# Kernel optimization log

Hardware: AMD Instinct MI355X
Metric: run time of the kernel (lower is better)

## Reference

```python
import jax, jax.numpy as jnp
import numpy as np

# --- reconstructed config / key constants (from init_kwargs) ---
SCALES = (8, 16, 32)                      # patch sizes tiling H, W
TEMPORAL_WINDOWS = (0, 250, 500, 750, 1000)
KEY_INT = 0x5D1CE5                        # deterministic int derived from watermark_key+model_id
BASE_STRENGTH = 0.05
HASH_MOD = 10007
TWO_PI = 6.2831853


def _watermark_bias_map(latent, timestep):
    """Vectorized equivalent of the per-scale / per-patch Python loops.

    For each scale p: tile HxW into (H/p)x(W/p) patches, pool latent over
    (batch, channel, patch) -> scalar per patch, combine with a keyed integer
    hash phase into g in [-1,1], scale by a per-(scale,timestep) strength, and
    paint the constant bias over each patch region (the spatial mask).
    Returns a [H, W] bias map broadcastable over [B, C, H, W].
    """
    B, C, H, W = latent.shape
    # temporal bucket (timestep is a static Python int)
    bucket = int(np.searchsorted(np.asarray(TEMPORAL_WINDOWS), timestep, side='right') - 1)
    total = jnp.zeros((H, W), dtype=latent.dtype)
    for p in SCALES:
        gh, gw = H // p, W // p
        # pooled features per patch: mean over batch, channels, and patch pixels -> [gh, gw]
        pooled = latent.reshape(B, C, gh, p, gw, p).mean(axis=(0, 1, 3, 5))
        # keyed hash phase per patch (top-left coords i*p, j*p)
        base = (KEY_INT * 2654435761 + p * 97 + bucket * 139) % HASH_MOD
        i = (jnp.arange(gh, dtype=jnp.int32) * (p * 131))[:, None]
        j = (jnp.arange(gw, dtype=jnp.int32) * (p * 137))[None, :]
        h = (base + i + j) % HASH_MOD                           # [gh, gw] int
        phase = h.astype(latent.dtype) * (TWO_PI / HASH_MOD)
        g = jnp.cos(pooled * 3.0 + phase)                       # g_value in [-1, 1]
        strength = np.float32(BASE_STRENGTH / np.sqrt(p) * np.exp(-timestep / 1000.0))
        # broadcast patch-constant bias over the full spatial mask region
        total = total + jnp.repeat(jnp.repeat(g * strength, p, axis=0), p, axis=1)
    return total


def setup_inputs() -> dict:
    key = jax.random.key(0)
    k1, k2 = jax.random.split(key)
    B, C, H, W = 64, 4, 256, 256
    noise = jax.random.normal(k1, (B, C, H, W), dtype=jnp.float32)
    latent = jax.random.normal(k2, (B, C, H, W), dtype=jnp.float32)
    return {"noise": noise, "latent": latent, "timestep": 500}


def reference(noise, latent, timestep):
    bias = _watermark_bias_map(latent, timestep)        # [H, W]
    return noise + bias[None, None, :, :]               # [B, C, H, W]
```

## Files before the change

### kernel.cpp

```cpp
#include <hip/hip_runtime.h>
#include <hip/hip_bf16.h>

static constexpr int KEY_MUL =
    (int)((6102245ULL * 2654435761ULL) % 10007ULL);
static constexpr int HASH_MOD = 10007;

typedef float f32x4 __attribute__((ext_vector_type(4)));

__global__ __launch_bounds__(256, 8) void pool_kernel32(
    const float* __restrict__ latent, float* __restrict__ ws_partial) {
  const int ch = blockIdx.x;
  const int pr = blockIdx.y >> 1;
  const int half = blockIdx.y & 1;
  const int t = threadIdx.x;
  const int cl = t & 31;
  const int rg = t >> 5;

  const float4* base = reinterpret_cast<const float4*>(latent);
  float4 v[8];
#pragma unroll
  for (int pl = 0; pl < 8; ++pl)
    v[pl] = base[(size_t)(ch * 8 + pl) * 16384 + (pr * 8 + rg) * 64 +
                 half * 32 + cl];
  float acc = 0.0f;
#pragma unroll
  for (int pl = 0; pl < 8; ++pl) acc += (v[pl].x + v[pl].y) + (v[pl].z + v[pl].w);
  acc += __shfl_xor(acc, 1, 64);

  __shared__ float lds[8][16];
  if ((cl & 1) == 0) lds[rg][cl >> 1] = acc;
  __syncthreads();
  if (t < 16) {
    float s = ((lds[0][t] + lds[1][t]) + (lds[2][t] + lds[3][t])) +
              ((lds[4][t] + lds[5][t]) + (lds[6][t] + lds[7][t]));
    ws_partial[(pr * 32 + half * 16 + t) * 32 + ch] = s;
  }
}

template <int NCH>
__global__ __launch_bounds__(256) void pool_kernel_legacy(
    const float* __restrict__ latent, float* __restrict__ ws_partial) {
  constexpr int PPC = 256 / NCH;
  const int pr = blockIdx.y, ch = blockIdx.x, t = threadIdx.x;
  const int cl = t & 63, rg = t >> 6;
  float acc = 0.0f;
  const float4* base = reinterpret_cast<const float4*>(latent);
#pragma unroll 8
  for (int pl = 0; pl < PPC; ++pl) {
    const float4* prow = base + (size_t)(ch * PPC + pl) * 16384;
#pragma unroll
    for (int rr = 0; rr < 2; ++rr) {
      float4 v = prow[(pr * 8 + rg + rr * 4) * 64 + cl];
      acc += (v.x + v.y) + (v.z + v.w);
    }
  }
  acc += __shfl_xor(acc, 1, 64);
  __shared__ float lds[4][32];
  if ((cl & 1) == 0) lds[rg][cl >> 1] = acc;
  __syncthreads();
  if (t < 32) {
    float s = (lds[0][t] + lds[1][t]) + (lds[2][t] + lds[3][t]);
    ws_partial[(pr * 32 + t) * NCH + ch] = s;
  }
}

template <int NCH>
__global__ __launch_bounds__(256, 8) void bias_add_kernel(
    const float* __restrict__ noise, const float* __restrict__ ws_partial,
    const int* __restrict__ tstep, float* __restrict__ out) {
  const int t = threadIdx.x;
  const int b = blockIdx.x;
  const int q = b & 7;

  __shared__ float s8[128];
  __shared__ float btot[128];

  const size_t slab = (size_t)(b >> 3) * 16384 + (size_t)q * 2048;
  const f32x4* __restrict__ n4 = reinterpret_cast<const f32x4*>(noise) + slab;
  f32x4* __restrict__ o4 = reinterpret_cast<f32x4*>(out) + slab;

  f32x4 v[8];
#pragma unroll
  for (int k = 0; k < 8; ++k) v[k] = n4[k * 256 + t];

  const int ts = *tstep;

  if (t < 128) {
    const int lr = t >> 5;
    const int lc = t & 31;
    const int patch = (4 * q + lr) * 32 + lc;
    float s = 0.0f;
    if constexpr (NCH >= 4) {
      const float4* p4 =
          reinterpret_cast<const float4*>(ws_partial) + patch * (NCH / 4);
#pragma unroll
      for (int c = 0; c < NCH / 4; ++c) {
        float4 w = p4[c];
        s += (w.x + w.y) + (w.z + w.w);
      }
    } else {
#pragma unroll
      for (int c = 0; c < NCH; ++c) s += ws_partial[patch * NCH + c];
    }
    s8[t] = s;
  }
  __syncthreads();

  if (t < 128) {
    const int lr = t >> 5;
    const int lc = t & 31;
    const int pr = 4 * q + lr;

    int bucket = -1;
    const int wins[5] = {0, 250, 500, 750, 1000};
#pragma unroll
    for (int k = 0; k < 5; ++k) bucket += (ts >= wins[k]) ? 1 : 0;

    const float expo = expf((float)(-ts) * 0.001f);
    const float phase_k = (float)(6.2831853 / 10007.0);

    float bias = 0.0f;
    {
      const int bb = (KEY_MUL + 8 * 97 + bucket * 139) % HASH_MOD;
      const int h = (bb + pr * (8 * 131) + lc * (8 * 137)) % HASH_MOD;
      const float pooled = s8[t] * (1.0f / 16384.0f);
      bias += cosf(pooled * 3.0f + (float)h * phase_k) *
              (0.0176776695296637f * expo);
    }
    {
      const int bb = (KEY_MUL + 16 * 97 + bucket * 139) % HASH_MOD;
      const int h =
          (bb + (pr >> 1) * (16 * 131) + (lc >> 1) * (16 * 137)) % HASH_MOD;
      const int r0 = (lr & ~1) * 32, c0 = lc & ~1;
      const float s = (s8[r0 + c0] + s8[r0 + c0 + 1]) +
                      (s8[r0 + 32 + c0] + s8[r0 + 32 + c0 + 1]);
      const float pooled = s * (1.0f / 65536.0f);
      bias += cosf(pooled * 3.0f + (float)h * phase_k) *
              (0.0125f * expo);
    }
    {
      const int bb = (KEY_MUL + 32 * 97 + bucket * 139) % HASH_MOD;
      const int h = (bb + q * (32 * 131) + (lc >> 2) * (32 * 137)) % HASH_MOD;
      const int c0 = lc & ~3;
      float s = 0.0f;
#pragma unroll
      for (int di = 0; di < 4; ++di)
#pragma unroll
        for (int dj = 0; dj < 4; ++dj) s += s8[di * 32 + c0 + dj];
      const float pooled = s * (1.0f / 262144.0f);
      bias += cosf(pooled * 3.0f + (float)h * phase_k) *
              (0.00883883476483184f * expo);
    }
    btot[t] = bias;
  }
  __syncthreads();

  {
    const int c8 = (t & 63) >> 1;
    const int r0 = t >> 6;
#pragma unroll
    for (int k = 0; k < 8; ++k) {
      const int lrow = k * 4 + r0;
      const float bs = btot[(lrow >> 3) * 32 + c8];
      f32x4 w = v[k];
      w.x += bs; w.y += bs; w.z += bs; w.w += bs;
      o4[k * 256 + t] = w;
    }
  }
}

extern "C" void kernel_launch(void* const* d_in, const int* in_sizes, int n_in,
                              void* d_out, int out_size, void* d_ws, size_t ws_size,
                              hipStream_t stream) {
  const float* noise  = (const float*)d_in[0];
  const float* latent = (const float*)d_in[1];
  const int*   tstep  = (const int*)d_in[2];
  float* out = (float*)d_out;
  float* ws  = (float*)d_ws;

  const size_t need32 = (size_t)(1024 * 32) * sizeof(float);
  const size_t need8  = (size_t)(1024 * 8) * sizeof(float);

  if (ws_size >= need32) {
    pool_kernel32<<<dim3(32, 64), 256, 0, stream>>>(latent, ws);
    bias_add_kernel<32><<<2048, 256, 0, stream>>>(noise, ws, tstep, out);
  } else if (ws_size >= need8) {
    pool_kernel_legacy<8><<<dim3(8, 32), 256, 0, stream>>>(latent, ws);
    bias_add_kernel<8><<<2048, 256, 0, stream>>>(noise, ws, tstep, out);
  } else {
    pool_kernel_legacy<1><<<dim3(1, 32), 256, 0, stream>>>(latent, ws);
    bias_add_kernel<1><<<2048, 256, 0, stream>>>(noise, ws, tstep, out);
  }
}
```

Measured before the change: 36.20 us.

## Double per-block work in bias-add kernel and use nontemporal loads

```diff
diff --git a/kernel.cpp b/kernel.cpp
--- a/kernel.cpp
+++ b/kernel.cpp
@@ -16,15 +16,17 @@
   const int cl = t & 31;
   const int rg = t >> 5;
 
-  const float4* base = reinterpret_cast<const float4*>(latent);
-  float4 v[8];
+  const f32x4* base = reinterpret_cast<const f32x4*>(latent);
+  f32x4 v[8];
 #pragma unroll
   for (int pl = 0; pl < 8; ++pl)
-    v[pl] = base[(size_t)(ch * 8 + pl) * 16384 + (pr * 8 + rg) * 64 +
-                 half * 32 + cl];
+    v[pl] = __builtin_nontemporal_load(
+        &base[(size_t)(ch * 8 + pl) * 16384 + (pr * 8 + rg) * 64 + half * 32 +
+              cl]);
   float acc = 0.0f;
 #pragma unroll
-  for (int pl = 0; pl < 8; ++pl) acc += (v[pl].x + v[pl].y) + (v[pl].z + v[pl].w);
+  for (int pl = 0; pl < 8; ++pl)
+    acc += (v[pl].x + v[pl].y) + (v[pl].z + v[pl].w);
   acc += __shfl_xor(acc, 1, 64);
 
   __shared__ float lds[8][16];
@@ -65,52 +67,57 @@
 }
 
 template <int NCH>
-__global__ __launch_bounds__(256, 8) void bias_add_kernel(
+__global__ __launch_bounds__(256, 4) void bias_add_kernel(
     const float* __restrict__ noise, const float* __restrict__ ws_partial,
     const int* __restrict__ tstep, float* __restrict__ out) {
   const int t = threadIdx.x;
   const int b = blockIdx.x;
-  const int q = b & 7;
-
-  __shared__ float s8[128];
-  __shared__ float btot[128];
-
-  const size_t slab = (size_t)(b >> 3) * 16384 + (size_t)q * 2048;
+  const int q = b & 3;
+  const int lr = t >> 5;
+  const int lc = t & 31;
+  const int pr = 8 * q + lr;
+
+  __shared__ float s8[256];
+  __shared__ float btot[256];
+
+  const int patch = pr * 32 + lc;
+  f32x4 pp[NCH >= 4 ? NCH / 4 : 1];
+  float pp1[NCH >= 4 ? 1 : NCH];
+  if constexpr (NCH >= 4) {
+    const f32x4* p4 =
+        reinterpret_cast<const f32x4*>(ws_partial) + patch * (NCH / 4);
+#pragma unroll
+    for (int c = 0; c < NCH / 4; ++c) pp[c] = p4[c];
+  } else {
+#pragma unroll
+    for (int c = 0; c < NCH; ++c) pp1[c] = ws_partial[patch * NCH + c];
+  }
+
+  const size_t slab = (size_t)(b >> 2) * 16384 + (size_t)q * 4096;
   const f32x4* __restrict__ n4 = reinterpret_cast<const f32x4*>(noise) + slab;
   f32x4* __restrict__ o4 = reinterpret_cast<f32x4*>(out) + slab;
-
-  f32x4 v[8];
-#pragma unroll
-  for (int k = 0; k < 8; ++k) v[k] = n4[k * 256 + t];
+  f32x4 v[16];
+#pragma unroll
+  for (int k = 0; k < 16; ++k)
+    v[k] = __builtin_nontemporal_load(&n4[k * 256 + t]);
 
   const int ts = *tstep;
 
-  if (t < 128) {
-    const int lr = t >> 5;
-    const int lc = t & 31;
-    const int patch = (4 * q + lr) * 32 + lc;
+  {
     float s = 0.0f;
     if constexpr (NCH >= 4) {
-      const float4* p4 =
-          reinterpret_cast<const float4*>(ws_partial) + patch * (NCH / 4);
-#pragma unroll
-      for (int c = 0; c < NCH / 4; ++c) {
-        float4 w = p4[c];
-        s += (w.x + w.y) + (w.z + w.w);
-      }
+#pragma unroll
+      for (int c = 0; c < NCH / 4; ++c)
+        s += (pp[c].x + pp[c].y) + (pp[c].z + pp[c].w);
     } else {
 #pragma unroll
-      for (int c = 0; c < NCH; ++c) s += ws_partial[patch * NCH + c];
+      for (int c = 0; c < NCH; ++c) s += pp1[c];
     }
     s8[t] = s;
   }
   __syncthreads();
 
-  if (t < 128) {
-    const int lr = t >> 5;
-    const int lc = t & 31;
-    const int pr = 4 * q + lr;
-
+  {
     int bucket = -1;
     const int wins[5] = {0, 250, 500, 750, 1000};
 #pragma unroll
@@ -140,13 +147,14 @@
     }
     {
       const int bb = (KEY_MUL + 32 * 97 + bucket * 139) % HASH_MOD;
-      const int h = (bb + q * (32 * 131) + (lc >> 2) * (32 * 137)) % HASH_MOD;
-      const int c0 = lc & ~3;
+      const int h =
+          (bb + (pr >> 2) * (32 * 131) + (lc >> 2) * (32 * 137)) % HASH_MOD;
+      const int r0 = (lr & ~3) * 32, c0 = lc & ~3;
       float s = 0.0f;
 #pragma unroll
       for (int di = 0; di < 4; ++di)
 #pragma unroll
-        for (int dj = 0; dj < 4; ++dj) s += s8[di * 32 + c0 + dj];
+        for (int dj = 0; dj < 4; ++dj) s += s8[r0 + di * 32 + c0 + dj];
       const float pooled = s * (1.0f / 262144.0f);
       bias += cosf(pooled * 3.0f + (float)h * phase_k) *
               (0.00883883476483184f * expo);
@@ -159,7 +167,7 @@
     const int c8 = (t & 63) >> 1;
     const int r0 = t >> 6;
 #pragma unroll
-    for (int k = 0; k < 8; ++k) {
+    for (int k = 0; k < 16; ++k) {
       const int lrow = k * 4 + r0;
       const float bs = btot[(lrow >> 3) * 32 + c8];
       f32x4 w = v[k];
@@ -179,16 +187,16 @@
   float* ws  = (float*)d_ws;
 
   const size_t need32 = (size_t)(1024 * 32) * sizeof(float);
-  const size_t need8  = (size_t)(1024 * 8) * sizeof(float);
+  const size_t need1  = (size_t)1024 * sizeof(float);
 
   if (ws_size >= need32) {
     pool_kernel32<<<dim3(32, 64), 256, 0, stream>>>(latent, ws);
-    bias_add_kernel<32><<<2048, 256, 0, stream>>>(noise, ws, tstep, out);
-  } else if (ws_size >= need8) {
-    pool_kernel_legacy<8><<<dim3(8, 32), 256, 0, stream>>>(latent, ws);
-    bias_add_kernel<8><<<2048, 256, 0, stream>>>(noise, ws, tstep, out);
+    bias_add_kernel<32><<<1024, 256, 0, stream>>>(noise, ws, tstep, out);
+  } else if (ws_size >= need1) {
+    pool_kernel_legacy<1><<<dim3(1, 32), 256, 0, stream>>>(latent, ws);
+    bias_add_kernel<1><<<1024, 256, 0, stream>>>(noise, ws, tstep, out);
   } else {
     pool_kernel_legacy<1><<<dim3(1, 32), 256, 0, stream>>>(latent, ws);
-    bias_add_kernel<1><<<2048, 256, 0, stream>>>(noise, ws, tstep, out);
-  }
-}
+    bias_add_kernel<1><<<1024, 256, 0, stream>>>(noise, ws, tstep, out);
+  }
+}
```

New measurement: 43.30 us. +19.6%, slower.
